# Kernel tuning notes

Measured on AMD Instinct MI355X. Metric: run time of the kernel, lower is better.

## Reference

```python
import jax, jax.numpy as jnp
import numpy as np

IN_FEATURES = 1024
OUT_FEATURES = 1024
GRID_SIZE = 5
SPLINE_ORDER = 3
GRID_RANGE = (-1.0, 1.0)


def make_grid():
    h = (GRID_RANGE[1] - GRID_RANGE[0]) / GRID_SIZE
    knots = jnp.arange(-SPLINE_ORDER, GRID_SIZE + SPLINE_ORDER + 1, dtype=jnp.float32) * h + GRID_RANGE[0]
    return jnp.broadcast_to(knots, (IN_FEATURES, knots.shape[0]))  # (in, 12)


def b_splines(x, knots, p):
    # x: (B, in); knots: (in, nk). Cox-de Boor recursion, degree p.
    xs = x[:, :, None]                                   # (B, in, 1)
    bases = ((xs >= knots[None, :, :-1]) & (xs < knots[None, :, 1:])).astype(x.dtype)
    for k in range(1, p + 1):
        den1 = knots[:, k:-1] - knots[:, :-(k + 1)]
        den1 = jnp.where(den1 == 0, jnp.float32(1e-8), den1)
        den2 = knots[:, k + 1:] - knots[:, 1:-k]
        den2 = jnp.where(den2 == 0, jnp.float32(1e-8), den2)
        term1 = (xs - knots[None, :, :-(k + 1)]) / den1[None] * bases[:, :, :-1]
        term2 = (knots[None, :, k + 1:] - xs) / den2[None] * bases[:, :, 1:]
        bases = term1 + term2
    return bases  # (B, in, grid_size + p)


def setup_inputs() -> dict:
    key = jax.random.key(0)
    k1, k2, k3, k4 = jax.random.split(key, 4)
    K = GRID_SIZE + SPLINE_ORDER
    x = jax.random.normal(k1, (4096, IN_FEATURES), dtype=jnp.float32)
    base_weight = jax.random.normal(k2, (OUT_FEATURES, IN_FEATURES), dtype=jnp.float32) * (1.0 / np.sqrt(IN_FEATURES))
    spline_weight = jax.random.normal(k3, (OUT_FEATURES, IN_FEATURES, K), dtype=jnp.float32) * 0.02
    spline_scaler = jax.random.normal(k4, (OUT_FEATURES, IN_FEATURES), dtype=jnp.float32) * (1.0 / np.sqrt(IN_FEATURES))
    grid = make_grid()
    return {"x": x, "base_weight": base_weight, "spline_weight": spline_weight,
            "spline_scaler": spline_scaler, "grid": grid}


def reference(x, base_weight, spline_weight, spline_scaler, grid):
    base_out = jax.nn.silu(x) @ base_weight.T                      # (B, out)
    bases = b_splines(x, grid, SPLINE_ORDER)                       # (B, in, K)
    scaled_sw = spline_weight * spline_scaler[:, :, None]          # (out, in, K)
    spline_out = jnp.einsum('bik,oik->bo', bases, scaled_sw)       # (B, out)
    return base_out + spline_out
```

## Files before the change

### kernel.cpp

```cpp
#include <hip/hip_runtime.h>
#include <hip/hip_bf16.h>
#include <cstdint>
#include <cstddef>

#define AS1 __attribute__((address_space(1)))
#define AS3 __attribute__((address_space(3)))

typedef __bf16 bf16;
typedef __bf16 bf16x8 __attribute__((ext_vector_type(8)));
typedef float f32x4 __attribute__((ext_vector_type(4)));

static constexpr int M_ROWS = 4096;
static constexpr int N_COLS = 1024;
static constexpr int IN_F   = 1024;
static constexpr int K2     = IN_F * 9;
static constexpr int BK     = 32;
static constexpr int KT_CNT = K2 / BK;

static constexpr int GBK = 64;
static constexpr int GKT = K2 / GBK;


__device__ __forceinline__ void bases8(float x, float w8[8]) {
  float mf = x * 2.5f + 5.5f;
  int   m  = (int)floorf(mf);
  float u  = mf - (float)m;
  float u2 = u * u, u3 = u2 * u;
  float omu = 1.0f - u;
  const float s = 1.0f / 6.0f;
  float p0 = u3 * s;
  float p1 = (-3.f*u3 + 3.f*u2 + 3.f*u + 1.f) * s;
  float p2 = (3.f*u3 - 6.f*u2 + 4.f) * s;
  float p3 = omu * omu * omu * s;
  bool in = (m >= 0) && (m < 11);
#pragma unroll
  for (int j = 0; j < 8; ++j) {
    float v = 0.0f;
    v = (j == m)     ? p0 : v;
    v = (j == m - 1) ? p1 : v;
    v = (j == m - 2) ? p2 : v;
    v = (j == m - 3) ? p3 : v;
    w8[j] = in ? v : 0.0f;
  }
}

__global__ void expand_a(const float* __restrict__ x, bf16* __restrict__ A,
                         int r0) {
  int gid = blockIdx.x * blockDim.x + threadIdx.x;
  int b = gid >> 10;
  int i = gid & 1023;
  float xv = x[(size_t)r0 * IN_F + (size_t)gid];

  A[(size_t)b * K2 + i] = (bf16)(xv / (1.0f + __expf(-xv)));

  float w8[8];
  bases8(xv, w8);
  bf16x8 outv;
#pragma unroll
  for (int j = 0; j < 8; ++j) outv[j] = (bf16)w8[j];
  *(bf16x8*)(A + (size_t)b * K2 + IN_F + (size_t)i * 8) = outv;
}

__global__ void make_bt(const float* __restrict__ bw, const float* __restrict__ sw,
                        const float* __restrict__ sc, bf16* __restrict__ BT) {
  int gid = blockIdx.x * blockDim.x + threadIdx.x;
  int o = gid >> 10;
  int i = gid & 1023;

  BT[(size_t)o * K2 + i] = (bf16)bw[gid];

  float scale = sc[gid];
  const float4* swp = (const float4*)(sw + (size_t)gid * 8);
  float4 a = swp[0], b4 = swp[1];
  float wv[8] = {a.x, a.y, a.z, a.w, b4.x, b4.y, b4.z, b4.w};
  bf16x8 r;
#pragma unroll
  for (int j = 0; j < 8; ++j) r[j] = (bf16)(wv[j] * scale);
  *(bf16x8*)(BT + (size_t)o * K2 + IN_F + (size_t)i * 8) = r;
}

__global__ __launch_bounds__(256, 2) void gemm_fused(
    const bf16* __restrict__ A, const bf16* __restrict__ BT,
    float* __restrict__ d0, float* __restrict__ d1,
    int r0, int mt_cnt, int kt_seg) {
  __shared__ bf16 As[2][128 * GBK];
  __shared__ bf16 Bs[2][128 * GBK];

  const int tid  = threadIdx.x;
  const int lane = tid & 63;
  const int w    = tid >> 6;

  const int bps = mt_cnt * 8;
  int b   = blockIdx.x;
  const int seg = b / bps;
  b -= seg * bps;
  const int row0 = (b % mt_cnt) * 128;
  const int col0 = (b / mt_cnt) * 128;
  float* __restrict__ dst = seg ? d1 : d0;
  const int kt0 = seg * kt_seg;

  const int srow = lane >> 3;
  const int sch  = ((lane & 7) ^ srow) * 8;

  const int r  = lane & 15;
  const int q  = lane >> 4;
  const int wm = (w >> 1) * 64;
  const int wn = (w & 1) * 64;
  const int kc0 = ((0 + q) ^ (r & 7)) * 8;
  const int kc1 = ((4 + q) ^ (r & 7)) * 8;

  const bf16* aB = A  + (size_t)row0 * K2;
  const bf16* bB = BT + (size_t)col0 * K2;

  f32x4 acc[4][4];
#pragma unroll
  for (int mt = 0; mt < 4; ++mt)
#pragma unroll
    for (int nt = 0; nt < 4; ++nt)
      acc[mt][nt] = f32x4{0.f, 0.f, 0.f, 0.f};

  auto stage = [&](int sbuf, int kt) {
#pragma unroll
    for (int t = 0; t < 4; ++t) {
      const int rg = w * 32 + t * 8;
      const bf16* ga = aB + (size_t)(rg + srow) * K2 + kt * GBK + sch;
      __builtin_amdgcn_global_load_lds((const AS1 void*)ga,
                                       (AS3 void*)&As[sbuf][rg * GBK], 16, 0, 0);
      const bf16* gb = bB + (size_t)(rg + srow) * K2 + kt * GBK + sch;
      __builtin_amdgcn_global_load_lds((const AS1 void*)gb,
                                       (AS3 void*)&Bs[sbuf][rg * GBK], 16, 0, 0);
    }
  };

  stage(0, kt0);
  int buf = 0;
  for (int i = 0; i < kt_seg; ++i) {
    if (i + 1 < kt_seg) {
      stage(buf ^ 1, kt0 + i + 1);
      asm volatile("s_waitcnt vmcnt(8)" ::: "memory");
    } else {
      asm volatile("s_waitcnt vmcnt(0)" ::: "memory");
    }
    __builtin_amdgcn_s_barrier();
    __builtin_amdgcn_sched_barrier(0);

    const bf16* as = As[buf];
    const bf16* bs = Bs[buf];

#pragma unroll
    for (int kk = 0; kk < 2; ++kk) {
      const int kc = kk ? kc1 : kc0;
      bf16x8 af[4], bfr[4];
#pragma unroll
      for (int mt = 0; mt < 4; ++mt)
        af[mt] = *(const bf16x8*)&as[(wm + mt * 16 + r) * GBK + kc];
#pragma unroll
      for (int nt = 0; nt < 4; ++nt)
        bfr[nt] = *(const bf16x8*)&bs[(wn + nt * 16 + r) * GBK + kc];
#pragma unroll
      for (int mt = 0; mt < 4; ++mt)
#pragma unroll
        for (int nt = 0; nt < 4; ++nt)
          acc[mt][nt] = __builtin_amdgcn_mfma_f32_16x16x32_bf16(
              af[mt], bfr[nt], acc[mt][nt], 0, 0, 0);
    }
    __builtin_amdgcn_s_barrier();
    buf ^= 1;
  }

#pragma unroll
  for (int mt = 0; mt < 4; ++mt)
#pragma unroll
    for (int nt = 0; nt < 4; ++nt)
#pragma unroll
      for (int k = 0; k < 4; ++k) {
        int row = r0 + row0 + wm + mt * 16 + q * 4 + k;
        int col = col0 + wn + nt * 16 + r;
        dst[(size_t)row * N_COLS + col] = acc[mt][nt][k];
      }
}

__global__ void reduce_add(const float* __restrict__ p0,
                           const float* __restrict__ p1,
                           float* __restrict__ out) {
  int i = blockIdx.x * blockDim.x + threadIdx.x;
  f32x4 a = ((const f32x4*)p0)[i];
  f32x4 b = ((const f32x4*)p1)[i];
  ((f32x4*)out)[i] = a + b;
}

__global__ __launch_bounds__(256) void kan_fused_fallback(
    const float* __restrict__ x, const float* __restrict__ bw,
    const float* __restrict__ sw, const float* __restrict__ sc,
    float* __restrict__ out) {
  __shared__ bf16 As[64 * BK];
  __shared__ bf16 Bs[128 * BK];
  const int tid  = threadIdx.x;
  const int lane = tid & 63;
  const int w    = tid >> 6;
  const int col0 = blockIdx.x * 128;
  const int row0 = blockIdx.y * 64;
  const int srow = tid >> 2, sq = tid & 3;
  const int r = lane & 15, q = lane >> 4, wn = w * 32;

  f32x4 acc[4][2];
#pragma unroll
  for (int mt = 0; mt < 4; ++mt)
#pragma unroll
    for (int nt = 0; nt < 2; ++nt) acc[mt][nt] = f32x4{0,0,0,0};

  for (int kt = 0; kt < KT_CNT; ++kt) {
    if (kt < 32) {
      const int cc = sq * 8;
      const float4* xp = (const float4*)(x + (size_t)(row0+srow)*IN_F + kt*BK + cc);
      float4 a = xp[0], b4 = xp[1];
      float xv[8] = {a.x,a.y,a.z,a.w,b4.x,b4.y,b4.z,b4.w};
      bf16x8 av;
#pragma unroll
      for (int j = 0; j < 8; ++j) av[j] = (bf16)(xv[j] / (1.0f + __expf(-xv[j])));
      *(bf16x8*)&As[srow * BK + cc] = av;
#pragma unroll
      for (int h = 0; h < 2; ++h) {
        const float4* bp = (const float4*)(bw + (size_t)(col0+h*64+srow)*IN_F + kt*BK + cc);
        float4 c0 = bp[0], c1 = bp[1];
        float bv[8] = {c0.x,c0.y,c0.z,c0.w,c1.x,c1.y,c1.z,c1.w};
        bf16x8 bb;
#pragma unroll
        for (int j = 0; j < 8; ++j) bb[j] = (bf16)bv[j];
        *(bf16x8*)&Bs[(h*64+srow)*BK + cc] = bb;
      }
    } else {
      const int i = (kt - 32) * 4 + sq;
      float xv = x[(size_t)(row0+srow)*IN_F + i];
      float w8[8]; bases8(xv, w8);
      bf16x8 av;
#pragma unroll
      for (int j = 0; j < 8; ++j) av[j] = (bf16)w8[j];
      *(bf16x8*)&As[srow * BK + sq * 8] = av;
#pragma unroll
      for (int h = 0; h < 2; ++h) {
        const int o = col0 + h*64 + srow;
        float s1 = sc[(size_t)o*IN_F + i];
        const float4* sp = (const float4*)(sw + ((size_t)o*IN_F + i)*8);
        float4 c0 = sp[0], c1 = sp[1];
        float wv[8] = {c0.x,c0.y,c0.z,c0.w,c1.x,c1.y,c1.z,c1.w};
        bf16x8 bb;
#pragma unroll
        for (int j = 0; j < 8; ++j) bb[j] = (bf16)(wv[j]*s1);
        *(bf16x8*)&Bs[(h*64+srow)*BK + sq*8] = bb;
      }
    }
    __syncthreads();
    bf16x8 af[4], bfr[2];
#pragma unroll
    for (int mt = 0; mt < 4; ++mt)
      af[mt] = *(const bf16x8*)&As[(mt*16+r)*BK + q*8];
#pragma unroll
    for (int nt = 0; nt < 2; ++nt)
      bfr[nt] = *(const bf16x8*)&Bs[(wn+nt*16+r)*BK + q*8];
#pragma unroll
    for (int mt = 0; mt < 4; ++mt)
#pragma unroll
      for (int nt = 0; nt < 2; ++nt)
        acc[mt][nt] = __builtin_amdgcn_mfma_f32_16x16x32_bf16(af[mt], bfr[nt], acc[mt][nt], 0,0,0);
    __syncthreads();
  }
#pragma unroll
  for (int mt = 0; mt < 4; ++mt)
#pragma unroll
    for (int nt = 0; nt < 2; ++nt)
#pragma unroll
      for (int k = 0; k < 4; ++k)
        out[(size_t)(row0+mt*16+q*4+k)*N_COLS + col0+wn+nt*16+r] = acc[mt][nt][k];
}

extern "C" void kernel_launch(void* const* d_in, const int* in_sizes, int n_in,
                              void* d_out, int out_size, void* d_ws, size_t ws_size,
                              hipStream_t stream) {
  const float* x    = (const float*)d_in[0];
  const float* bw   = (const float*)d_in[1];
  const float* sw   = (const float*)d_in[2];
  const float* sc   = (const float*)d_in[3];
  float* out = (float*)d_out;

  const size_t BT_BYTES  = (size_t)N_COLS * K2 * sizeof(bf16);
  const size_t ROW_BYTES = (size_t)K2 * sizeof(bf16);
  const size_t A_BYTES   = (size_t)M_ROWS * ROW_BYTES;
  const size_t OUT_BYTES = (size_t)M_ROWS * N_COLS * sizeof(float);

  if (BT_BYTES + A_BYTES + 2 * OUT_BYTES <= ws_size) {
    bf16*  BT    = (bf16*)d_ws;
    bf16*  Aslab = BT + (size_t)N_COLS * K2;
    float* P0    = (float*)((char*)d_ws + BT_BYTES + A_BYTES);
    float* P1    = P0 + (size_t)M_ROWS * N_COLS;
    make_bt<<<(N_COLS * IN_F) / 256, 256, 0, stream>>>(bw, sw, sc, BT);
    expand_a<<<(M_ROWS * IN_F) / 256, 256, 0, stream>>>(x, Aslab, 0);
    gemm_fused<<<2 * (M_ROWS / 128) * (N_COLS / 128), 256, 0, stream>>>(
        Aslab, BT, P0, P1, 0, M_ROWS / 128, GKT / 2);
    reduce_add<<<(M_ROWS * N_COLS) / (4 * 256), 256, 0, stream>>>(P0, P1, out);
  } else {
    int SL = 0;
    for (int cand = 4096; cand >= 128; cand >>= 1)
      if (BT_BYTES + (size_t)cand * ROW_BYTES <= ws_size) { SL = cand; break; }
    if (SL) {
      bf16* BT    = (bf16*)d_ws;
      bf16* Aslab = BT + (size_t)N_COLS * K2;
      make_bt<<<(N_COLS * IN_F) / 256, 256, 0, stream>>>(bw, sw, sc, BT);
      for (int r0 = 0; r0 < M_ROWS; r0 += SL) {
        expand_a<<<(SL * IN_F) / 256, 256, 0, stream>>>(x, Aslab, r0);
        gemm_fused<<<(SL / 128) * (N_COLS / 128), 256, 0, stream>>>(
            Aslab, BT, out, out, r0, SL / 128, GKT);
      }
    } else {
      kan_fused_fallback<<<dim3(N_COLS / 128, M_ROWS / 64), 256, 0, stream>>>(
          x, bw, sw, sc, out);
    }
  }
  (void)in_sizes; (void)n_in; (void)out_size;
}
```

Baseline: 204.4 us.

## Use 256x256-tile 512-thread GEMM with up-to-4-way split-K and N-plane reduction

Adds a new GEMM kernel that computes 256x256 output tiles with 8 waves per block, double-buffered LDS loads, and raised wave priority around the MFMA loops. It replaces the 128x128 two-way split-K path with a split-K of up to 4, where each segment writes its own partial plane. A generalized reduction kernel then sums all partial planes. The larger tiles reuse each loaded operand more and the extra split keeps about one block per CU. In exchange the partial-sum traffic grows, and the bigger tiles use a lot of LDS and registers at occupancy 1.

```diff
diff --git a/kernel.cpp b/kernel.cpp
--- a/kernel.cpp
+++ b/kernel.cpp
@@ -79,6 +79,108 @@
   *(bf16x8*)(BT + (size_t)o * K2 + IN_F + (size_t)i * 8) = r;
 }
 
+__global__ __launch_bounds__(512, 1) void gemm256(
+    const bf16* __restrict__ A, const bf16* __restrict__ BT,
+    float* __restrict__ P, int kt_seg) {
+  __shared__ bf16 As[2][256 * GBK];
+  __shared__ bf16 Bs[2][256 * GBK];
+
+  const int tid  = threadIdx.x;
+  const int lane = tid & 63;
+  const int w    = tid >> 6;
+
+  const int b     = blockIdx.x;
+  const int mtile = b & 15;
+  const int np    = (b >> 4) & 3;
+  const int seg   = b >> 6;
+  const int row0  = mtile * 256;
+  const int col0  = np * 256;
+  const int kt0   = seg * kt_seg;
+  float* __restrict__ dst = P + (size_t)seg * M_ROWS * N_COLS;
+
+  const int srow = lane >> 3;
+  const int sch  = ((lane & 7) ^ srow) * 8;
+
+  const int r  = lane & 15;
+  const int q  = lane >> 4;
+  const int wm = (w >> 2) * 128;
+  const int wn = (w & 3) * 64;
+  const int kc0 = ((0 + q) ^ (r & 7)) * 8;
+  const int kc1 = ((4 + q) ^ (r & 7)) * 8;
+
+  const bf16* aB = A  + (size_t)row0 * K2;
+  const bf16* bB = BT + (size_t)col0 * K2;
+
+  f32x4 acc[8][4];
+#pragma unroll
+  for (int mt = 0; mt < 8; ++mt)
+#pragma unroll
+    for (int nt = 0; nt < 4; ++nt)
+      acc[mt][nt] = f32x4{0.f, 0.f, 0.f, 0.f};
+
+  auto stage = [&](int sbuf, int kt) {
+#pragma unroll
+    for (int t = 0; t < 4; ++t) {
+      const int rg = w * 32 + t * 8;
+      const bf16* ga = aB + (size_t)(rg + srow) * K2 + kt * GBK + sch;
+      __builtin_amdgcn_global_load_lds((const AS1 void*)ga,
+                                       (AS3 void*)&As[sbuf][rg * GBK], 16, 0, 0);
+      const bf16* gb = bB + (size_t)(rg + srow) * K2 + kt * GBK + sch;
+      __builtin_amdgcn_global_load_lds((const AS1 void*)gb,
+                                       (AS3 void*)&Bs[sbuf][rg * GBK], 16, 0, 0);
+    }
+  };
+
+  stage(0, kt0);
+  int buf = 0;
+  for (int i = 0; i < kt_seg; ++i) {
+    if (i + 1 < kt_seg) {
+      stage(buf ^ 1, kt0 + i + 1);
+      asm volatile("s_waitcnt vmcnt(8)" ::: "memory");
+    } else {
+      asm volatile("s_waitcnt vmcnt(0)" ::: "memory");
+    }
+    __builtin_amdgcn_s_barrier();
+    __builtin_amdgcn_sched_barrier(0);
+
+    const bf16* as = As[buf];
+    const bf16* bs = Bs[buf];
+
+#pragma unroll
+    for (int kk = 0; kk < 2; ++kk) {
+      const int kc = kk ? kc1 : kc0;
+      bf16x8 af[8], bfr[4];
+#pragma unroll
+      for (int mt = 0; mt < 8; ++mt)
+        af[mt] = *(const bf16x8*)&as[(wm + mt * 16 + r) * GBK + kc];
+#pragma unroll
+      for (int nt = 0; nt < 4; ++nt)
+        bfr[nt] = *(const bf16x8*)&bs[(wn + nt * 16 + r) * GBK + kc];
+      __builtin_amdgcn_s_setprio(1);
+#pragma unroll
+      for (int mt = 0; mt < 8; ++mt)
+#pragma unroll
+        for (int nt = 0; nt < 4; ++nt)
+          acc[mt][nt] = __builtin_amdgcn_mfma_f32_16x16x32_bf16(
+              af[mt], bfr[nt], acc[mt][nt], 0, 0, 0);
+      __builtin_amdgcn_s_setprio(0);
+    }
+    __builtin_amdgcn_s_barrier();
+    buf ^= 1;
+  }
+
+#pragma unroll
+  for (int mt = 0; mt < 8; ++mt)
+#pragma unroll
+    for (int nt = 0; nt < 4; ++nt)
+#pragma unroll
+      for (int k = 0; k < 4; ++k) {
+        int row = row0 + wm + mt * 16 + q * 4 + k;
+        int col = col0 + wn + nt * 16 + r;
+        dst[(size_t)row * N_COLS + col] = acc[mt][nt][k];
+      }
+}
+
 __global__ __launch_bounds__(256, 2) void gemm_fused(
     const bf16* __restrict__ A, const bf16* __restrict__ BT,
     float* __restrict__ d0, float* __restrict__ d1,
@@ -101,7 +203,6 @@
 
   const int srow = lane >> 3;
   const int sch  = ((lane & 7) ^ srow) * 8;
-
   const int r  = lane & 15;
   const int q  = lane >> 4;
   const int wm = (w >> 1) * 64;
@@ -180,13 +281,14 @@
       }
 }
 
-__global__ void reduce_add(const float* __restrict__ p0,
-                           const float* __restrict__ p1,
-                           float* __restrict__ out) {
-  int i = blockIdx.x * blockDim.x + threadIdx.x;
-  f32x4 a = ((const f32x4*)p0)[i];
-  f32x4 b = ((const f32x4*)p1)[i];
-  ((f32x4*)out)[i] = a + b;
+__global__ void reduce_addN(const float* __restrict__ P,
+                            float* __restrict__ out, int segs) {
+  size_t i = (size_t)blockIdx.x * blockDim.x + threadIdx.x;
+  const f32x4* p = (const f32x4*)P;
+  const size_t plane = (size_t)M_ROWS * N_COLS / 4;
+  f32x4 a = p[i];
+  for (int s = 1; s < segs; ++s) a += p[(size_t)s * plane + i];
+  ((f32x4*)out)[i] = a;
 }
 
 __global__ __launch_bounds__(256) void kan_fused_fallback(
@@ -288,16 +390,20 @@
   const size_t A_BYTES   = (size_t)M_ROWS * ROW_BYTES;
   const size_t OUT_BYTES = (size_t)M_ROWS * N_COLS * sizeof(float);
 
-  if (BT_BYTES + A_BYTES + 2 * OUT_BYTES <= ws_size) {
+  int S = 0;
+  for (int c = 4; c >= 2; --c)
+    if (GKT % c == 0 && BT_BYTES + A_BYTES + (size_t)c * OUT_BYTES <= ws_size) {
+      S = c; break;
+    }
+
+  if (S >= 2) {
     bf16*  BT    = (bf16*)d_ws;
     bf16*  Aslab = BT + (size_t)N_COLS * K2;
-    float* P0    = (float*)((char*)d_ws + BT_BYTES + A_BYTES);
-    float* P1    = P0 + (size_t)M_ROWS * N_COLS;
+    float* P     = (float*)((char*)d_ws + BT_BYTES + A_BYTES);
     make_bt<<<(N_COLS * IN_F) / 256, 256, 0, stream>>>(bw, sw, sc, BT);
     expand_a<<<(M_ROWS * IN_F) / 256, 256, 0, stream>>>(x, Aslab, 0);
-    gemm_fused<<<2 * (M_ROWS / 128) * (N_COLS / 128), 256, 0, stream>>>(
-        Aslab, BT, P0, P1, 0, M_ROWS / 128, GKT / 2);
-    reduce_add<<<(M_ROWS * N_COLS) / (4 * 256), 256, 0, stream>>>(P0, P1, out);
+    gemm256<<<S * 64, 512, 0, stream>>>(Aslab, BT, P, GKT / S);
+    reduce_addN<<<(M_ROWS * N_COLS) / (4 * 256), 256, 0, stream>>>(P, out, S);
   } else {
     int SL = 0;
     for (int cand = 4096; cand >= 128; cand >>= 1)
```

After: 208.2 us. Within noise of the previous version (+1.8%).
